# Optimization experiments

Hardware: AMD Instinct MI355X
Metric: run time of the kernel (lower is better)

Reference implementation:

```python
import jax, jax.numpy as jnp
import numpy as np

THRESHOLD = 0.8
B, D, H, C = 8192, 4096, 8192, 2

def _mlp(x, w1, b1, w2, b2):
    h = jax.nn.relu(x @ w1 + b1)
    return h @ w2 + b2

def setup_inputs() -> dict:
    key = jax.random.key(0)
    ks = jax.random.split(key, 5)
    s1 = 1.0 / np.sqrt(D)
    s2 = 1.0 / np.sqrt(H)
    return {
        "x": jax.random.normal(ks[0], (B, D), dtype=jnp.float32),
        "t_w1": jax.random.normal(ks[1], (D, H), dtype=jnp.float32) * s1,
        "t_b1": jnp.zeros((H,), dtype=jnp.float32),
        "t_w2": jax.random.normal(ks[2], (H, C), dtype=jnp.float32) * s2,
        "t_b2": jnp.zeros((C,), dtype=jnp.float32),
        "f_w1": jax.random.normal(ks[3], (D, H), dtype=jnp.float32) * s1,
        "f_b1": jnp.zeros((H,), dtype=jnp.float32),
        "f_w2": jax.random.normal(ks[4], (H, C), dtype=jnp.float32) * s2,
        "f_b2": jnp.zeros((C,), dtype=jnp.float32),
    }

def reference(x, t_w1, t_b1, t_w2, t_b2, f_w1, f_b1, f_w2, f_b2):
    # Texture expert logits [B, C]
    t_out = _mlp(x, t_w1, t_b1, t_w2, t_b2)
    # Confidence = max softmax prob per row
    conf = jnp.max(jax.nn.softmax(t_out, axis=1), axis=1)
    low_conf = conf < THRESHOLD  # [B] bool
    # Frequency expert logits (jit-friendly: compute for all rows, select per row;
    # identical math to torch's masked gather/scatter)
    f_out = _mlp(x, f_w1, f_b1, f_w2, f_b2)
    return jnp.where(low_conf[:, None], f_out, t_out)
```

## Files before the change

kernel.cpp:

```cpp
#include <hip/hip_runtime.h>
#include <stdint.h>

typedef unsigned short u16;
typedef _Float16 f16x8 __attribute__((ext_vector_type(8)));
typedef float f32x4 __attribute__((ext_vector_type(4)));

#define B_ROWS 8192
#define K_DIM  4096
#define H_DIM  8192
#define W_SCALE 64.0f
#define INV_W_SCALE 0.015625f

#define ARR_STRIDE (33554432u)

__device__ __forceinline__ u16 f2h_bits(float f) {
  _Float16 h = (_Float16)f;
  return __builtin_bit_cast(u16, h);
}
__device__ __forceinline__ float h2f(u16 u) {
  return (float)__builtin_bit_cast(_Float16, u);
}

typedef __attribute__((address_space(1))) void gvoid_t;
typedef __attribute__((address_space(3))) void lvoid_t;
#define GLOAD_LDS16(gp, lp) \
  __builtin_amdgcn_global_load_lds((gvoid_t*)(gp), (lvoid_t*)(lp), 16, 0, 0)

__global__ void split_x_kernel(const float4* __restrict__ x,
                               ushort4* __restrict__ hi,
                               ushort4* __restrict__ lo, int n4) {
  int i = blockIdx.x * blockDim.x + threadIdx.x;
  if (i >= n4) return;
  float4 v = x[i];
  ushort4 h, l;
  h.x = f2h_bits(v.x); l.x = f2h_bits(v.x - h2f(h.x));
  h.y = f2h_bits(v.y); l.y = f2h_bits(v.y - h2f(h.y));
  h.z = f2h_bits(v.z); l.z = f2h_bits(v.z - h2f(h.z));
  h.w = f2h_bits(v.w); l.w = f2h_bits(v.w - h2f(h.w));
  hi[i] = h; lo[i] = l;
}

__global__ void transpose_split_kernel(const float* __restrict__ w,
                                       u16* __restrict__ hi, u16* __restrict__ lo,
                                       int rows, int cols) {
  __shared__ float tile[32][33];
  int c0 = blockIdx.x * 32, r0 = blockIdx.y * 32;
  int tx = threadIdx.x, ty = threadIdx.y;
  #pragma unroll
  for (int j = 0; j < 4; ++j)
    tile[ty + j*8][tx] = w[(size_t)(r0 + ty + j*8) * cols + c0 + tx];
  __syncthreads();
  #pragma unroll
  for (int j = 0; j < 4; ++j) {
    int oc = c0 + ty + j*8;
    float v = tile[tx][ty + j*8] * W_SCALE;
    u16 h = f2h_bits(v);
    size_t oidx = (size_t)oc * rows + r0 + tx;
    hi[oidx] = h;
    if (lo) lo[oidx] = f2h_bits(v - h2f(h));
  }
}

__global__ void init_parts_kernel(float* __restrict__ tp, float* __restrict__ fp,
                                  const float* __restrict__ tb2,
                                  const float* __restrict__ fb2) {
  int i = blockIdx.x * blockDim.x + threadIdx.x;
  if (i < 2 * B_ROWS) { tp[i] = tb2[i & 1]; fp[i] = fb2[i & 1]; }
}

__device__ __forceinline__ void epilogue(
    const f32x4 (&acc)[4][4], const float* __restrict__ b1,
    const float* __restrict__ w2, float* __restrict__ part,
    int mbase, int nbase, int r)
{
  float b1v[4], w20[4], w21[4];
  #pragma unroll
  for (int t = 0; t < 4; ++t) {
    int n = nbase + t * 16;
    b1v[t] = b1[n];
    w20[t] = w2[2*n];
    w21[t] = w2[2*n + 1];
  }
  #pragma unroll
  for (int tm = 0; tm < 4; ++tm) {
    #pragma unroll
    for (int v = 0; v < 4; ++v) {
      float s0 = 0.f, s1 = 0.f;
      #pragma unroll
      for (int tn = 0; tn < 4; ++tn) {
        float h = fmaxf(fmaf(acc[tm][tn][v], INV_W_SCALE, b1v[tn]), 0.f);
        s0 = fmaf(h, w20[tn], s0);
        s1 = fmaf(h, w21[tn], s1);
      }
      #pragma unroll
      for (int off = 1; off < 16; off <<= 1) {
        s0 += __shfl_xor(s0, off, 64);
        s1 += __shfl_xor(s1, off, 64);
      }
      if (r == 0) {
        int m = mbase + tm * 16 + v;
        atomicAdd(&part[2*m],     s0);
        atomicAdd(&part[2*m + 1], s1);
      }
    }
  }
}

#define LBUF 28672
__global__ __launch_bounds__(512, 2) void fused_mlp_kernel(
    const u16* __restrict__ ws16,
    const float* __restrict__ tb1, const float* __restrict__ tw2,
    const float* __restrict__ fb1, const float* __restrict__ fw2,
    float* __restrict__ tp, float* __restrict__ fp)
{
  __shared__ __align__(16) u16 lds[2 * LBUF];

  const int tid  = threadIdx.x;
  const int lane = tid & 63;
  const int wave = tid >> 6;
  const int wm = wave >> 1;
  const int wn = wave & 1;
  const int q  = lane >> 4;
  const int r  = lane & 15;

  const int L  = blockIdx.x;
  const int s  = L >> 3;
  const int bm = (s >> 5) * 4 + ((s >> 3) & 3);
  const int bn = (L & 7) * 8 + (s & 7);

  unsigned goff[7];
  int loff[7];
  #pragma unroll
  for (int j = 0; j < 7; ++j) {
    int gid = wave * 7 + j;
    unsigned arr; int g, lbase; bool isA;
    if (gid < 16)      { arr = 0; g = gid;      lbase = 0;     isA = true;  }
    else if (gid < 32) { arr = 1; g = gid - 16; lbase = 8192;  isA = true;  }
    else if (gid < 40) { arr = 2; g = gid - 32; lbase = 16384; isA = false; }
    else if (gid < 48) { arr = 3; g = gid - 40; lbase = 20480; isA = false; }
    else               { arr = 4; g = gid - 48; lbase = 24576; isA = false; }
    unsigned row = (isA ? (unsigned)bm * 256u : (unsigned)bn * 128u) + g * 16 + r;
    goff[j] = arr * ARR_STRIDE + row * (unsigned)K_DIM + q * 8;
    loff[j] = lbase + g * 512;
  }

  f32x4 at[4][4], af[4][4];
  #pragma unroll
  for (int i = 0; i < 4; ++i)
    #pragma unroll
    for (int j = 0; j < 4; ++j) {
      at[i][j] = (f32x4){0.f, 0.f, 0.f, 0.f};
      af[i][j] = (f32x4){0.f, 0.f, 0.f, 0.f};
    }

  #pragma unroll
  for (int j = 0; j < 7; ++j)
    GLOAD_LDS16(ws16 + goff[j], &lds[loff[j]]);

  int p = 0;
  for (int kk = 0; kk < K_DIM / 32; ++kk) {
    __syncthreads();

    if (kk + 1 < K_DIM / 32) {
      const unsigned ka = (unsigned)(kk + 1) * 32u;
      const int lb = (p ^ 1) * LBUF;
      #pragma unroll
      for (int j = 0; j < 7; ++j)
        GLOAD_LDS16(ws16 + goff[j] + ka, &lds[lb + loff[j]]);
    }

    const int base = p * LBUF;
    f16x8 ah[4], bb[4], tmp[4];
    #pragma unroll
    for (int t = 0; t < 4; ++t) {
      ah[t] = *reinterpret_cast<const f16x8*>(&lds[base + (wm*4 + t)*512 + lane*8]);
      bb[t] = *reinterpret_cast<const f16x8*>(&lds[base + 16384 + (wn*4 + t)*512 + lane*8]);
    }
    #pragma unroll
    for (int tm = 0; tm < 4; ++tm)
      #pragma unroll
      for (int tn = 0; tn < 4; ++tn)
        at[tm][tn] = __builtin_amdgcn_mfma_f32_16x16x32_f16(ah[tm], bb[tn], at[tm][tn], 0, 0, 0);

    #pragma unroll
    for (int t = 0; t < 4; ++t)
      tmp[t] = *reinterpret_cast<const f16x8*>(&lds[base + 8192 + (wm*4 + t)*512 + lane*8]);
    #pragma unroll
    for (int tm = 0; tm < 4; ++tm)
      #pragma unroll
      for (int tn = 0; tn < 4; ++tn)
        at[tm][tn] = __builtin_amdgcn_mfma_f32_16x16x32_f16(tmp[tm], bb[tn], at[tm][tn], 0, 0, 0);

    #pragma unroll
    for (int t = 0; t < 4; ++t)
      tmp[t] = *reinterpret_cast<const f16x8*>(&lds[base + 20480 + (wn*4 + t)*512 + lane*8]);
    #pragma unroll
    for (int tm = 0; tm < 4; ++tm)
      #pragma unroll
      for (int tn = 0; tn < 4; ++tn)
        at[tm][tn] = __builtin_amdgcn_mfma_f32_16x16x32_f16(ah[tm], tmp[tn], at[tm][tn], 0, 0, 0);

    #pragma unroll
    for (int t = 0; t < 4; ++t)
      tmp[t] = *reinterpret_cast<const f16x8*>(&lds[base + 24576 + (wn*4 + t)*512 + lane*8]);
    #pragma unroll
    for (int tm = 0; tm < 4; ++tm)
      #pragma unroll
      for (int tn = 0; tn < 4; ++tn)
        af[tm][tn] = __builtin_amdgcn_mfma_f32_16x16x32_f16(ah[tm], tmp[tn], af[tm][tn], 0, 0, 0);

    p ^= 1;
  }

  const int mbase = bm * 256 + wm * 64 + q * 4;
  const int nbase = bn * 128 + wn * 64 + r;
  epilogue(at, tb1, tw2, tp, mbase, nbase, r);
  epilogue(af, fb1, fw2, fp, mbase, nbase, r);
}

__global__ void select_kernel(const float* __restrict__ tp, const float* __restrict__ fp,
                              float* __restrict__ out) {
  int m = blockIdx.x * blockDim.x + threadIdx.x;
  if (m >= B_ROWS) return;
  float a = tp[2*m], b = tp[2*m + 1];
  float conf = 1.0f / (1.0f + expf(-fabsf(a - b)));
  bool low = conf < 0.8f;
  out[2*m]     = low ? fp[2*m]     : a;
  out[2*m + 1] = low ? fp[2*m + 1] : b;
}

extern "C" void kernel_launch(void* const* d_in, const int* in_sizes, int n_in,
                              void* d_out, int out_size, void* d_ws, size_t ws_size,
                              hipStream_t stream) {
  const float* x    = (const float*)d_in[0];
  const float* t_w1 = (const float*)d_in[1];
  const float* t_b1 = (const float*)d_in[2];
  const float* t_w2 = (const float*)d_in[3];
  const float* t_b2 = (const float*)d_in[4];
  const float* f_w1 = (const float*)d_in[5];
  const float* f_b1 = (const float*)d_in[6];
  const float* f_w2 = (const float*)d_in[7];
  const float* f_b2 = (const float*)d_in[8];
  float* out = (float*)d_out;

  const size_t SZ = (size_t)B_ROWS * K_DIM * sizeof(u16);
  const size_t NEED = 5 * SZ + 2 * (size_t)(2 * B_ROWS) * sizeof(float);
  if (ws_size < NEED) return;

  char* ws = (char*)d_ws;
  u16* x_hi   = (u16*)(ws);
  u16* x_lo   = (u16*)(ws + SZ);
  u16* twT_hi = (u16*)(ws + 2 * SZ);
  u16* twT_lo = (u16*)(ws + 3 * SZ);
  u16* fwT_hi = (u16*)(ws + 4 * SZ);
  float* t_part = (float*)(ws + 5 * SZ);
  float* f_part = t_part + 2 * B_ROWS;

  split_x_kernel<<<(B_ROWS * K_DIM / 4 + 255) / 256, 256, 0, stream>>>(
      (const float4*)x, (ushort4*)x_hi, (ushort4*)x_lo, B_ROWS * K_DIM / 4);
  dim3 tb(32, 8);
  transpose_split_kernel<<<dim3(H_DIM / 32, K_DIM / 32), tb, 0, stream>>>(
      t_w1, twT_hi, twT_lo, K_DIM, H_DIM);
  transpose_split_kernel<<<dim3(H_DIM / 32, K_DIM / 32), tb, 0, stream>>>(
      f_w1, fwT_hi, nullptr, K_DIM, H_DIM);
  init_parts_kernel<<<(2 * B_ROWS + 255) / 256, 256, 0, stream>>>(
      t_part, f_part, t_b2, f_b2);

  fused_mlp_kernel<<<(B_ROWS / 256) * (H_DIM / 128), 512, 0, stream>>>(
      x_hi, t_b1, t_w2, f_b1, f_w2, t_part, f_part);

  select_kernel<<<(B_ROWS + 255) / 256, 256, 0, stream>>>(t_part, f_part, out);
}
```

Baseline: 2.854 ms.

## Deepen K-loop prefetch to two stages with explicit vmcnt waits and setprio

Restructures the main GEMM K-loop so global-to-LDS loads for step kk+2 are issued after the current step's compute. Partial vmcnt waits keep one load batch in flight, replacing the full __syncthreads at the top of each iteration. Each MFMA cluster is wrapped in s_barrier/sched_barrier plus s_setprio so waves interleave LDS reads and MFMA work across the two waves per SIMD. This adds several barriers per iteration, which could cost time if the waves' phases don't line up.

```diff
diff --git a/kernel.cpp b/kernel.cpp
--- a/kernel.cpp
+++ b/kernel.cpp
@@ -107,6 +107,7 @@
 }
 
 #define LBUF 28672
+#define NK   (K_DIM / 32)
 __global__ __launch_bounds__(512, 2) void fused_mlp_kernel(
     const u16* __restrict__ ws16,
     const float* __restrict__ tb1, const float* __restrict__ tw2,
@@ -156,60 +157,91 @@
   #pragma unroll
   for (int j = 0; j < 7; ++j)
     GLOAD_LDS16(ws16 + goff[j], &lds[loff[j]]);
-
-  int p = 0;
-  for (int kk = 0; kk < K_DIM / 32; ++kk) {
-    __syncthreads();
-
-    if (kk + 1 < K_DIM / 32) {
-      const unsigned ka = (unsigned)(kk + 1) * 32u;
-      const int lb = (p ^ 1) * LBUF;
-      #pragma unroll
-      for (int j = 0; j < 7; ++j)
-        GLOAD_LDS16(ws16 + goff[j] + ka, &lds[lb + loff[j]]);
-    }
-
-    const int base = p * LBUF;
+  #pragma unroll
+  for (int j = 0; j < 7; ++j)
+    GLOAD_LDS16(ws16 + goff[j] + 32u, &lds[LBUF + loff[j]]);
+  asm volatile("s_waitcnt vmcnt(7)" ::: "memory");
+  __builtin_amdgcn_s_barrier();
+  __builtin_amdgcn_sched_barrier(0);
+
+  for (int kk = 0; kk < NK; ++kk) {
+    const int base = (kk & 1) * LBUF;
     f16x8 ah[4], bb[4], tmp[4];
+
     #pragma unroll
     for (int t = 0; t < 4; ++t) {
       ah[t] = *reinterpret_cast<const f16x8*>(&lds[base + (wm*4 + t)*512 + lane*8]);
       bb[t] = *reinterpret_cast<const f16x8*>(&lds[base + 16384 + (wn*4 + t)*512 + lane*8]);
     }
+    __builtin_amdgcn_s_barrier();
+    __builtin_amdgcn_sched_barrier(0);
+    __builtin_amdgcn_s_setprio(1);
     #pragma unroll
     for (int tm = 0; tm < 4; ++tm)
       #pragma unroll
       for (int tn = 0; tn < 4; ++tn)
         at[tm][tn] = __builtin_amdgcn_mfma_f32_16x16x32_f16(ah[tm], bb[tn], at[tm][tn], 0, 0, 0);
+    __builtin_amdgcn_s_setprio(0);
+    __builtin_amdgcn_s_barrier();
+    __builtin_amdgcn_sched_barrier(0);
 
     #pragma unroll
     for (int t = 0; t < 4; ++t)
       tmp[t] = *reinterpret_cast<const f16x8*>(&lds[base + 8192 + (wm*4 + t)*512 + lane*8]);
+    __builtin_amdgcn_s_barrier();
+    __builtin_amdgcn_sched_barrier(0);
+    __builtin_amdgcn_s_setprio(1);
     #pragma unroll
     for (int tm = 0; tm < 4; ++tm)
       #pragma unroll
       for (int tn = 0; tn < 4; ++tn)
         at[tm][tn] = __builtin_amdgcn_mfma_f32_16x16x32_f16(tmp[tm], bb[tn], at[tm][tn], 0, 0, 0);
+    __builtin_amdgcn_s_setprio(0);
+    __builtin_amdgcn_s_barrier();
+    __builtin_amdgcn_sched_barrier(0);
 
     #pragma unroll
     for (int t = 0; t < 4; ++t)
       tmp[t] = *reinterpret_cast<const f16x8*>(&lds[base + 20480 + (wn*4 + t)*512 + lane*8]);
+    __builtin_amdgcn_s_barrier();
+    __builtin_amdgcn_sched_barrier(0);
+    __builtin_amdgcn_s_setprio(1);
     #pragma unroll
     for (int tm = 0; tm < 4; ++tm)
       #pragma unroll
       for (int tn = 0; tn < 4; ++tn)
         at[tm][tn] = __builtin_amdgcn_mfma_f32_16x16x32_f16(ah[tm], tmp[tn], at[tm][tn], 0, 0, 0);
+    __builtin_amdgcn_s_setprio(0);
+    __builtin_amdgcn_s_barrier();
+    __builtin_amdgcn_sched_barrier(0);
 
     #pragma unroll
     for (int t = 0; t < 4; ++t)
       tmp[t] = *reinterpret_cast<const f16x8*>(&lds[base + 24576 + (wn*4 + t)*512 + lane*8]);
+    __builtin_amdgcn_s_barrier();
+    __builtin_amdgcn_sched_barrier(0);
+    __builtin_amdgcn_s_setprio(1);
     #pragma unroll
     for (int tm = 0; tm < 4; ++tm)
       #pragma unroll
       for (int tn = 0; tn < 4; ++tn)
         af[tm][tn] = __builtin_amdgcn_mfma_f32_16x16x32_f16(ah[tm], tmp[tn], af[tm][tn], 0, 0, 0);
-
-    p ^= 1;
+    __builtin_amdgcn_s_setprio(0);
+
+    if (kk + 2 < NK) {
+      const unsigned ka = (unsigned)(kk + 2) * 32u;
+      const int lb = (kk & 1) * LBUF;
+      #pragma unroll
+      for (int j = 0; j < 7; ++j)
+        GLOAD_LDS16(ws16 + goff[j] + ka, &lds[lb + loff[j]]);
+      asm volatile("s_waitcnt vmcnt(7)" ::: "memory");
+      __builtin_amdgcn_s_barrier();
+      __builtin_amdgcn_sched_barrier(0);
+    } else if (kk + 1 < NK) {
+      asm volatile("s_waitcnt vmcnt(0)" ::: "memory");
+      __builtin_amdgcn_s_barrier();
+      __builtin_amdgcn_sched_barrier(0);
+    }
   }
 
   const int mbase = bm * 256 + wm * 64 + q * 4;
```

After: 3.066 ms. +7.4%, slower.
